# Optimization experiments

Measured on AMD Instinct MI355X. Metric: run time of the kernel, lower is better.

Reference implementation:

```python
import jax, jax.numpy as jnp
import numpy as np

VOCAB = 12288
EMB = 128
EXP_ALPHA = 0.75
X_MAX = 100.0


def setup_inputs() -> dict:
    key = jax.random.key(0)
    k1, k2, k3, k4, k5 = jax.random.split(key, 5)
    return {
        "matriz_coocurrencias": jax.random.uniform(k1, (VOCAB, VOCAB), dtype=jnp.float32) * 50.0,
        "target_emb": jax.random.normal(k2, (VOCAB, EMB), dtype=jnp.float32),
        "context_emb": jax.random.normal(k3, (VOCAB, EMB), dtype=jnp.float32),
        "target_bias": jax.random.normal(k4, (VOCAB, 1), dtype=jnp.float32),
        "context_bias": jax.random.normal(k5, (VOCAB, 1), dtype=jnp.float32),
    }


def reference(matriz_coocurrencias, target_emb, context_emb, target_bias, context_bias):
    # dots = transpose(target @ context^T) == context @ target^T; dots[i, j] = c_i . t_j
    dots = jnp.matmul(context_emb, target_emb.T)  # [V, V]
    # + target_bias^T broadcasts over rows (bias of column word j),
    # + context_bias broadcasts over columns (bias of row word i)
    diff = dots + target_bias.T + context_bias - jnp.log1p(matriz_coocurrencias)
    # f(x) = clip((x / x_max)^alpha, 0, 1)
    weight = jnp.clip(jnp.power(matriz_coocurrencias / X_MAX, EXP_ALPHA), 0.0, 1.0)
    return jnp.sum(weight * diff * diff)
```

## Files before the change

kernel.cpp:

```cpp
#include <hip/hip_runtime.h>

#define VOCAB 12288
#define EMB 128
#define NBLK ((VOCAB / 128) * (VOCAB / 128))

typedef unsigned short u16;
typedef __bf16 bf16x8 __attribute__((ext_vector_type(8)));
typedef float f32x4 __attribute__((ext_vector_type(4)));

#define AS1 __attribute__((address_space(1)))
#define AS3 __attribute__((address_space(3)))

__device__ __forceinline__ u16 f2bf(float f) {
    unsigned u = __float_as_uint(f);
    u += 0x7FFF + ((u >> 16) & 1);
    return (u16)(u >> 16);
}

__device__ __forceinline__ void load_lds16(const void* g, void* l) {
    __builtin_amdgcn_global_load_lds((AS1 void*)const_cast<void*>(g),
                                     (AS3 void*)l, 16, 0, 0);
}

__device__ __forceinline__ float hw_exp2(float x) { return __builtin_amdgcn_exp2f(x); }
__device__ __forceinline__ float hw_log2(float x) { return __builtin_amdgcn_logf(x); }

__global__ __launch_bounds__(256) void glove_prep(
        const float* __restrict__ tgt, const float* __restrict__ ctx,
        u16* __restrict__ tgtb, u16* __restrict__ ctxb, float* __restrict__ out) {
    int idx = blockIdx.x * 256 + threadIdx.x;
    if (idx == 0) out[0] = 0.0f;
    const int N4 = (VOCAB * EMB) / 4;
    const float4* __restrict__ s;
    u16* __restrict__ d;
    int k = idx;
    if (k < N4) { s = (const float4*)tgt; d = tgtb; }
    else        { k -= N4; s = (const float4*)ctx; d = ctxb; }
    float4 v = s[k];
    unsigned lo = (unsigned)f2bf(v.x) | ((unsigned)f2bf(v.y) << 16);
    unsigned hi = (unsigned)f2bf(v.z) | ((unsigned)f2bf(v.w) << 16);
    ((uint2*)d)[k] = make_uint2(lo, hi);
}

__global__ __launch_bounds__(256) void glove_main(
        const float* __restrict__ X,
        const u16* __restrict__ ctxb, const u16* __restrict__ tgtb,
        const float* __restrict__ tb, const float* __restrict__ cb,
        float* __restrict__ out, float* __restrict__ partial) {
    __shared__ __bf16 smA[128 * EMB];
    __shared__ __bf16 smB[128 * EMB];

    const int tid  = threadIdx.x;
    const int lane = tid & 63;
    const int wave = tid >> 6;
    const int quad = lane >> 4;
    const int ln   = lane & 15;

    int bid = blockIdx.x;
    int xcd = bid & 7;
    int idx = bid >> 3;
    int by  = xcd * 12 + (idx / 96);
    int bx  = idx % 96;

    const int bi = by * 128;
    const int bj = bx * 128;

    const u16* gA = ctxb + (size_t)bi * EMB;
    const u16* gB = tgtb + (size_t)bj * EMB;

#pragma unroll
    for (int p = 0; p < 8; ++p) {
        int base = p * 256 + wave * 64;
        int L    = base + lane;
        int row  = L >> 4;
        int c    = (L & 15) ^ (row & 15);
        load_lds16(gA + row * EMB + c * 8, smA + base * 8);
        load_lds16(gB + row * EMB + c * 8, smB + base * 8);
    }
    __syncthreads();

    const int m_off = (wave & 1) * 64;
    const int n_off = (wave >> 1) * 64;

    f32x4 acc[4][4];
#pragma unroll
    for (int m = 0; m < 4; ++m)
#pragma unroll
        for (int n = 0; n < 4; ++n)
            acc[m][n] = (f32x4){0.f, 0.f, 0.f, 0.f};

#pragma unroll
    for (int s = 0; s < 4; ++s) {
        bf16x8 af[4], bf[4];
#pragma unroll
        for (int m = 0; m < 4; ++m) {
            int row = m_off + m * 16 + ln;
            int cp  = (s * 4 + quad) ^ (row & 15);
            af[m] = *(const bf16x8*)(smA + row * EMB + cp * 8);
        }
#pragma unroll
        for (int n = 0; n < 4; ++n) {
            int row = n_off + n * 16 + ln;
            int cp  = (s * 4 + quad) ^ (row & 15);
            bf[n] = *(const bf16x8*)(smB + row * EMB + cp * 8);
        }
#pragma unroll
        for (int m = 0; m < 4; ++m)
#pragma unroll
            for (int n = 0; n < 4; ++n)
                acc[m][n] = __builtin_amdgcn_mfma_f32_16x16x32_bf16(
                                af[m], bf[n], acc[m][n], 0, 0, 0);
    }

    const int gi0 = bi + m_off;
    const int gj0 = bj + n_off;

    float tbv[4];
#pragma unroll
    for (int n = 0; n < 4; ++n) tbv[n] = tb[gj0 + n * 16 + ln];

    const float LN2 = 0.69314718055994531f;
    float sum = 0.0f;
#pragma unroll
    for (int m = 0; m < 4; ++m) {
#pragma unroll
        for (int r = 0; r < 4; ++r) {
            int i = gi0 + m * 16 + quad * 4 + r;
            float cbi = cb[i];
            const float* xp = X + (size_t)i * VOCAB + gj0 + ln;
#pragma unroll
            for (int n = 0; n < 4; ++n) {
                float x  = __builtin_nontemporal_load(xp + n * 16);
                float d  = acc[m][n][r] + tbv[n] + cbi - LN2 * hw_log2(1.0f + x);
                float xs = x * 0.01f;
                float w  = hw_exp2(0.75f * hw_log2(xs));
                w = fminf(w, 1.0f);
                sum = fmaf(w * d, d, sum);
            }
        }
    }

#pragma unroll
    for (int off = 32; off > 0; off >>= 1) sum += __shfl_down(sum, off);

    __syncthreads();
    float* red = (float*)smA;
    if (lane == 0) red[wave] = sum;
    __syncthreads();
    if (tid == 0) {
        float v = red[0] + red[1] + red[2] + red[3];
        if (partial) partial[blockIdx.x] = v;
        else         atomicAdd(out, v);
    }
}

__global__ __launch_bounds__(256) void glove_reduce(
        const float* __restrict__ partial, float* __restrict__ out) {
    int tid = threadIdx.x;
    float s = 0.0f;
    const float4* p4 = (const float4*)partial;
    for (int k = tid; k < NBLK / 4; k += 256) {
        float4 v = p4[k];
        s += v.x + v.y + v.z + v.w;
    }
#pragma unroll
    for (int off = 32; off > 0; off >>= 1) s += __shfl_down(s, off);
    __shared__ float red[4];
    if ((tid & 63) == 0) red[tid >> 6] = s;
    __syncthreads();
    if (tid == 0) out[0] = red[0] + red[1] + red[2] + red[3];
}

extern "C" void kernel_launch(void* const* d_in, const int* in_sizes, int n_in,
                              void* d_out, int out_size, void* d_ws, size_t ws_size,
                              hipStream_t stream) {
    const float* X   = (const float*)d_in[0];
    const float* tgt = (const float*)d_in[1];
    const float* ctx = (const float*)d_in[2];
    const float* tb  = (const float*)d_in[3];
    const float* cb  = (const float*)d_in[4];
    float* out = (float*)d_out;

    u16* tgtb = (u16*)d_ws;
    u16* ctxb = tgtb + (size_t)VOCAB * EMB;

    const size_t emb_bytes = (size_t)VOCAB * EMB * sizeof(u16) * 2;
    float* partial = nullptr;
    if (ws_size >= emb_bytes + (size_t)NBLK * sizeof(float))
        partial = (float*)((char*)d_ws + emb_bytes);

    glove_prep<<<dim3(2 * (VOCAB * EMB / 4) / 256), 256, 0, stream>>>(
        tgt, ctx, tgtb, ctxb, out);
    glove_main<<<dim3(NBLK), 256, 0, stream>>>(
        X, ctxb, tgtb, tb, cb, out, partial);
    if (partial)
        glove_reduce<<<dim3(1), 256, 0, stream>>>(partial, out);
}
```

Measured before the change: 825.0 us.

## Retile GloVe kernel to 32x512 blocks with LDS-staged async X loads

```diff
diff --git a/kernel.cpp b/kernel.cpp
--- a/kernel.cpp
+++ b/kernel.cpp
@@ -2,7 +2,11 @@
 
 #define VOCAB 12288
 #define EMB 128
-#define NBLK ((VOCAB / 128) * (VOCAB / 128))
+#define TI 32
+#define TJ 512
+#define NBI (VOCAB / TI)
+#define NBJ (VOCAB / TJ)
+#define NBLK (NBI * NBJ)
 
 typedef unsigned short u16;
 typedef __bf16 bf16x8 __attribute__((ext_vector_type(8)));
@@ -42,13 +46,13 @@
     ((uint2*)d)[k] = make_uint2(lo, hi);
 }
 
-__global__ __launch_bounds__(256) void glove_main(
+__global__ __launch_bounds__(512, 4) void glove_main(
         const float* __restrict__ X,
         const u16* __restrict__ ctxb, const u16* __restrict__ tgtb,
         const float* __restrict__ tb, const float* __restrict__ cb,
         float* __restrict__ out, float* __restrict__ partial) {
-    __shared__ __bf16 smA[128 * EMB];
-    __shared__ __bf16 smB[128 * EMB];
+    __shared__ __bf16 smA[TI * EMB];
+    __shared__ float  smX[TI * TJ];
 
     const int tid  = threadIdx.x;
     const int lane = tid & 63;
@@ -59,78 +63,84 @@
     int bid = blockIdx.x;
     int xcd = bid & 7;
     int idx = bid >> 3;
-    int by  = xcd * 12 + (idx / 96);
-    int bx  = idx % 96;
-
-    const int bi = by * 128;
-    const int bj = bx * 128;
-
-    const u16* gA = ctxb + (size_t)bi * EMB;
-    const u16* gB = tgtb + (size_t)bj * EMB;
-
-#pragma unroll
-    for (int p = 0; p < 8; ++p) {
-        int base = p * 256 + wave * 64;
-        int L    = base + lane;
-        int row  = L >> 4;
-        int c    = (L & 15) ^ (row & 15);
-        load_lds16(gA + row * EMB + c * 8, smA + base * 8);
-        load_lds16(gB + row * EMB + c * 8, smB + base * 8);
+    int jb  = xcd * 3 + (idx / NBI);
+    int ib  = idx % NBI;
+
+    const int bi = ib * TI;
+    const int bj = jb * TJ;
+
+    {
+        int row = tid >> 4;
+        int c   = tid & 15;
+        uint4 v = *(const uint4*)(ctxb + (size_t)(bi + row) * EMB + c * 8);
+        int cs  = c ^ (row & 15);
+        *(uint4*)(smA + row * EMB + cs * 8) = v;
     }
     __syncthreads();
 
-    const int m_off = (wave & 1) * 64;
-    const int n_off = (wave >> 1) * 64;
-
-    f32x4 acc[4][4];
-#pragma unroll
-    for (int m = 0; m < 4; ++m)
+    const int jw = wave * 64;
+
+    f32x4 acc[2][4];
+#pragma unroll
+    for (int m = 0; m < 2; ++m)
 #pragma unroll
         for (int n = 0; n < 4; ++n)
             acc[m][n] = (f32x4){0.f, 0.f, 0.f, 0.f};
 
 #pragma unroll
     for (int s = 0; s < 4; ++s) {
-        bf16x8 af[4], bf[4];
-#pragma unroll
-        for (int m = 0; m < 4; ++m) {
-            int row = m_off + m * 16 + ln;
-            int cp  = (s * 4 + quad) ^ (row & 15);
+        bf16x8 af[2], bf[4];
+#pragma unroll
+        for (int m = 0; m < 2; ++m) {
+            int row = m * 16 + ln;
+            int cp  = (s * 4 + quad) ^ ln;
             af[m] = *(const bf16x8*)(smA + row * EMB + cp * 8);
         }
 #pragma unroll
         for (int n = 0; n < 4; ++n) {
-            int row = n_off + n * 16 + ln;
-            int cp  = (s * 4 + quad) ^ (row & 15);
-            bf[n] = *(const bf16x8*)(smB + row * EMB + cp * 8);
+            int grow = bj + jw + n * 16 + ln;
+            bf[n] = *(const bf16x8*)(tgtb + (size_t)grow * EMB + (s * 4 + quad) * 8);
         }
 #pragma unroll
-        for (int m = 0; m < 4; ++m)
+        for (int m = 0; m < 2; ++m)
 #pragma unroll
             for (int n = 0; n < 4; ++n)
                 acc[m][n] = __builtin_amdgcn_mfma_f32_16x16x32_bf16(
                                 af[m], bf[n], acc[m][n], 0, 0, 0);
     }
 
-    const int gi0 = bi + m_off;
-    const int gj0 = bj + n_off;
+    const float* gX = X + (size_t)bi * VOCAB + bj;
+#pragma unroll
+    for (int t = 0; t < 8; ++t) {
+        int g    = wave * 8 + t;
+        int row  = g >> 1;
+        int half = g & 1;
+        int c    = half * 64 + lane;
+        int cs   = c ^ (((row >> 2) & 1) << 2);
+        load_lds16(gX + (size_t)row * VOCAB + cs * 4, smX + g * 256);
+    }
+    asm volatile("s_waitcnt vmcnt(0)" ::: "memory");
+    __builtin_amdgcn_s_barrier();
 
     float tbv[4];
 #pragma unroll
-    for (int n = 0; n < 4; ++n) tbv[n] = tb[gj0 + n * 16 + ln];
+    for (int n = 0; n < 4; ++n) tbv[n] = tb[bj + jw + n * 16 + ln];
 
     const float LN2 = 0.69314718055994531f;
     float sum = 0.0f;
 #pragma unroll
-    for (int m = 0; m < 4; ++m) {
+    for (int m = 0; m < 2; ++m) {
 #pragma unroll
         for (int r = 0; r < 4; ++r) {
-            int i = gi0 + m * 16 + quad * 4 + r;
-            float cbi = cb[i];
-            const float* xp = X + (size_t)i * VOCAB + gj0 + ln;
+            int il = m * 16 + quad * 4 + r;
+            float cbi = cb[bi + il];
+            const float* xrow = smX + il * TJ;
+            int swz = ((il >> 2) & 1) << 2;
 #pragma unroll
             for (int n = 0; n < 4; ++n) {
-                float x  = __builtin_nontemporal_load(xp + n * 16);
+                int jl = jw + n * 16 + ln;
+                int cr = (jl >> 2) ^ swz;
+                float x  = xrow[(cr << 2) + (jl & 3)];
                 float d  = acc[m][n][r] + tbv[n] + cbi - LN2 * hw_log2(1.0f + x);
                 float xs = x * 0.01f;
                 float w  = hw_exp2(0.75f * hw_log2(xs));
@@ -143,12 +153,13 @@
 #pragma unroll
     for (int off = 32; off > 0; off >>= 1) sum += __shfl_down(sum, off);
 
-    __syncthreads();
     float* red = (float*)smA;
     if (lane == 0) red[wave] = sum;
     __syncthreads();
     if (tid == 0) {
-        float v = red[0] + red[1] + red[2] + red[3];
+        float v = 0.f;
+#pragma unroll
+        for (int w2 = 0; w2 < 8; ++w2) v += red[w2];
         if (partial) partial[blockIdx.x] = v;
         else         atomicAdd(out, v);
     }
@@ -191,7 +202,7 @@
 
     glove_prep<<<dim3(2 * (VOCAB * EMB / 4) / 256), 256, 0, stream>>>(
         tgt, ctx, tgtb, ctxb, out);
-    glove_main<<<dim3(NBLK), 256, 0, stream>>>(
+    glove_main<<<dim3(NBLK), 512, 0, stream>>>(
         X, ctxb, tgtb, tb, cb, out, partial);
     if (partial)
         glove_reduce<<<dim3(1), 256, 0, stream>>>(partial, out);
```

Result: slower. 851.9 us (+3.3%).

## Restructure into 16-row strips streaming target embeddings with vectorized X loads

Applied to the files above, without the earlier changes.

```diff
diff --git a/kernel.cpp b/kernel.cpp
--- a/kernel.cpp
+++ b/kernel.cpp
@@ -2,24 +2,19 @@
 
 #define VOCAB 12288
 #define EMB 128
-#define NBLK ((VOCAB / 128) * (VOCAB / 128))
+#define TI 16
+#define NSTRIP (VOCAB / TI)
+#define WCOLS (VOCAB / 4)
+#define NCHUNK (WCOLS / 256)
 
 typedef unsigned short u16;
 typedef __bf16 bf16x8 __attribute__((ext_vector_type(8)));
 typedef float f32x4 __attribute__((ext_vector_type(4)));
 
-#define AS1 __attribute__((address_space(1)))
-#define AS3 __attribute__((address_space(3)))
-
 __device__ __forceinline__ u16 f2bf(float f) {
     unsigned u = __float_as_uint(f);
     u += 0x7FFF + ((u >> 16) & 1);
     return (u16)(u >> 16);
-}
-
-__device__ __forceinline__ void load_lds16(const void* g, void* l) {
-    __builtin_amdgcn_global_load_lds((AS1 void*)const_cast<void*>(g),
-                                     (AS3 void*)l, 16, 0, 0);
 }
 
 __device__ __forceinline__ float hw_exp2(float x) { return __builtin_amdgcn_exp2f(x); }
@@ -42,13 +37,13 @@
     ((uint2*)d)[k] = make_uint2(lo, hi);
 }
 
-__global__ __launch_bounds__(256) void glove_main(
+__global__ __launch_bounds__(256, 3) void glove_main(
         const float* __restrict__ X,
         const u16* __restrict__ ctxb, const u16* __restrict__ tgtb,
         const float* __restrict__ tb, const float* __restrict__ cb,
         float* __restrict__ out, float* __restrict__ partial) {
-    __shared__ __bf16 smA[128 * EMB];
-    __shared__ __bf16 smB[128 * EMB];
+    __shared__ __bf16 smA[TI * EMB];
+    __shared__ float red[4];
 
     const int tid  = threadIdx.x;
     const int lane = tid & 63;
@@ -56,82 +51,57 @@
     const int quad = lane >> 4;
     const int ln   = lane & 15;
 
-    int bid = blockIdx.x;
-    int xcd = bid & 7;
-    int idx = bid >> 3;
-    int by  = xcd * 12 + (idx / 96);
-    int bx  = idx % 96;
+    const int bi = blockIdx.x * TI;
 
-    const int bi = by * 128;
-    const int bj = bx * 128;
-
-    const u16* gA = ctxb + (size_t)bi * EMB;
-    const u16* gB = tgtb + (size_t)bj * EMB;
-
-#pragma unroll
-    for (int p = 0; p < 8; ++p) {
-        int base = p * 256 + wave * 64;
-        int L    = base + lane;
-        int row  = L >> 4;
-        int c    = (L & 15) ^ (row & 15);
-        load_lds16(gA + row * EMB + c * 8, smA + base * 8);
-        load_lds16(gB + row * EMB + c * 8, smB + base * 8);
+    {
+        int row = tid >> 4;
+        int c   = tid & 15;
+        uint4 v = *(const uint4*)(ctxb + (size_t)(bi + row) * EMB + c * 8);
+        *(uint4*)(smA + row * EMB + (c ^ row) * 8) = v;
     }
     __syncthreads();
 
-    const int m_off = (wave & 1) * 64;
-    const int n_off = (wave >> 1) * 64;
+    bf16x8 bf[4];
+#pragma unroll
+    for (int s = 0; s < 4; ++s) {
+        int cp = (s * 4 + quad) ^ ln;
+        bf[s] = *(const bf16x8*)(smA + ln * EMB + cp * 8);
+    }
 
-    f32x4 acc[4][4];
+    const float cbi = cb[bi + ln];
+    const float LN2 = 0.69314718055994531f;
+    float sum = 0.0f;
+
+    const int jw = wave * WCOLS;
+
+    for (int ch = 0; ch < NCHUNK; ++ch) {
+        const int j0 = jw + ch * 256;
+
+        f32x4 acc[16];
 #pragma unroll
-    for (int m = 0; m < 4; ++m)
-#pragma unroll
-        for (int n = 0; n < 4; ++n)
-            acc[m][n] = (f32x4){0.f, 0.f, 0.f, 0.f};
+        for (int n = 0; n < 16; ++n) acc[n] = (f32x4){0.f, 0.f, 0.f, 0.f};
 
 #pragma unroll
-    for (int s = 0; s < 4; ++s) {
-        bf16x8 af[4], bf[4];
+        for (int n = 0; n < 16; ++n) {
+            const u16* ap = tgtb + (size_t)(j0 + n * 16 + ln) * EMB;
 #pragma unroll
-        for (int m = 0; m < 4; ++m) {
-            int row = m_off + m * 16 + ln;
-            int cp  = (s * 4 + quad) ^ (row & 15);
-            af[m] = *(const bf16x8*)(smA + row * EMB + cp * 8);
+            for (int s = 0; s < 4; ++s) {
+                bf16x8 af = *(const bf16x8*)(ap + (s * 4 + quad) * 8);
+                acc[n] = __builtin_amdgcn_mfma_f32_16x16x32_bf16(
+                             af, bf[s], acc[n], 0, 0, 0);
+            }
         }
+
+        const float* xrow = X + (size_t)(bi + ln) * VOCAB + j0 + quad * 4;
+        const float* tbp  = tb + j0 + quad * 4;
 #pragma unroll
-        for (int n = 0; n < 4; ++n) {
-            int row = n_off + n * 16 + ln;
-            int cp  = (s * 4 + quad) ^ (row & 15);
-            bf[n] = *(const bf16x8*)(smB + row * EMB + cp * 8);
-        }
+        for (int n = 0; n < 16; ++n) {
+            f32x4 xq  = __builtin_nontemporal_load((const f32x4*)(xrow + n * 16));
+            f32x4 tb4 = *(const f32x4*)(tbp + n * 16);
 #pragma unroll
-        for (int m = 0; m < 4; ++m)
-#pragma unroll
-            for (int n = 0; n < 4; ++n)
-                acc[m][n] = __builtin_amdgcn_mfma_f32_16x16x32_bf16(
-                                af[m], bf[n], acc[m][n], 0, 0, 0);
-    }
-
-    const int gi0 = bi + m_off;
-    const int gj0 = bj + n_off;
-
-    float tbv[4];
-#pragma unroll
-    for (int n = 0; n < 4; ++n) tbv[n] = tb[gj0 + n * 16 + ln];
-
-    const float LN2 = 0.69314718055994531f;
-    float sum = 0.0f;
-#pragma unroll
-    for (int m = 0; m < 4; ++m) {
-#pragma unroll
-        for (int r = 0; r < 4; ++r) {
-            int i = gi0 + m * 16 + quad * 4 + r;
-            float cbi = cb[i];
-            const float* xp = X + (size_t)i * VOCAB + gj0 + ln;
-#pragma unroll
-            for (int n = 0; n < 4; ++n) {
-                float x  = __builtin_nontemporal_load(xp + n * 16);
-                float d  = acc[m][n][r] + tbv[n] + cbi - LN2 * hw_log2(1.0f + x);
+            for (int r = 0; r < 4; ++r) {
+                float x  = xq[r];
+                float d  = acc[n][r] + tb4[r] + cbi - LN2 * hw_log2(1.0f + x);
                 float xs = x * 0.01f;
                 float w  = hw_exp2(0.75f * hw_log2(xs));
                 w = fminf(w, 1.0f);
@@ -143,8 +113,6 @@
 #pragma unroll
     for (int off = 32; off > 0; off >>= 1) sum += __shfl_down(sum, off);
 
-    __syncthreads();
-    float* red = (float*)smA;
     if (lane == 0) red[wave] = sum;
     __syncthreads();
     if (tid == 0) {
@@ -159,7 +127,7 @@
     int tid = threadIdx.x;
     float s = 0.0f;
     const float4* p4 = (const float4*)partial;
-    for (int k = tid; k < NBLK / 4; k += 256) {
+    for (int k = tid; k < NSTRIP / 4; k += 256) {
         float4 v = p4[k];
         s += v.x + v.y + v.z + v.w;
     }
@@ -186,12 +154,12 @@
 
     const size_t emb_bytes = (size_t)VOCAB * EMB * sizeof(u16) * 2;
     float* partial = nullptr;
-    if (ws_size >= emb_bytes + (size_t)NBLK * sizeof(float))
+    if (ws_size >= emb_bytes + (size_t)NSTRIP * sizeof(float))
         partial = (float*)((char*)d_ws + emb_bytes);
 
     glove_prep<<<dim3(2 * (VOCAB * EMB / 4) / 256), 256, 0, stream>>>(
         tgt, ctx, tgtb, ctxb, out);
-    glove_main<<<dim3(NBLK), 256, 0, stream>>>(
+    glove_main<<<dim3(NSTRIP), 256, 0, stream>>>(
         X, ctxb, tgtb, tb, cb, out, partial);
     if (partial)
         glove_reduce<<<dim3(1), 256, 0, stream>>>(partial, out);
```

New measurement: 1.105 ms. +33.9%, slower.
